# Optimization experiments

Hardware: AMD Instinct MI355X
Metric: run time of the kernel (lower is better)

## Reference

```python
import jax, jax.numpy as jnp
import numpy as np

B, N, S, D1, D2 = 8, 8192, 2048, 128, 256
MLP = [256, 128]
IN_CH = D1 + D2
EPS_INTERP = 1e-8
EPS_BN = 1e-5


def setup_inputs() -> dict:
    key = jax.random.key(0)
    ks = jax.random.split(key, 12)
    inp = {
        "xyz1": jax.random.normal(ks[0], (B, 3, N), dtype=jnp.float32),
        "xyz2": jax.random.normal(ks[1], (B, 3, S), dtype=jnp.float32),
        "points1": jax.random.normal(ks[2], (B, D1, N), dtype=jnp.float32),
        "points2": jax.random.normal(ks[3], (B, D2, S), dtype=jnp.float32),
    }
    # Conv1d(k=1) weights are [out, in]; BN has gamma/beta per channel.
    last = IN_CH
    for i, oc in enumerate(MLP):
        inp[f"W{i}"] = jax.random.normal(ks[4 + 2 * i], (oc, last), dtype=jnp.float32) * (1.0 / np.sqrt(last))
        inp[f"b{i}"] = jnp.zeros((oc,), dtype=jnp.float32)
        inp[f"g{i}"] = jnp.ones((oc,), dtype=jnp.float32)
        inp[f"be{i}"] = jnp.zeros((oc,), dtype=jnp.float32)
        last = oc
    return inp


def _interpolate(xyz1, xyz2, points2):
    # xyz1: [B,3,N] -> [B,N,3]; xyz2: [B,3,S] -> [B,S,3]; points2: [B,D2,S] -> [B,S,D2]
    x1 = jnp.transpose(xyz1, (0, 2, 1))
    x2 = jnp.transpose(xyz2, (0, 2, 1))
    p2 = jnp.transpose(points2, (0, 2, 1))
    # squared distances [B,N,S]
    dists = (jnp.sum(x1 * x1, -1)[:, :, None]
             - 2.0 * jnp.einsum("bnc,bsc->bns", x1, x2)
             + jnp.sum(x2 * x2, -1)[:, None, :])
    neg_d, idx = jax.lax.top_k(-dists, 3)         # 3 nearest neighbors
    d = -neg_d                                     # [B,N,3]
    recip = 1.0 / (d + EPS_INTERP)
    weight = recip / jnp.sum(recip, axis=2, keepdims=True)
    gathered = jax.vmap(lambda p, i: p[i])(p2, idx)   # [B,N,3,D2]
    return jnp.sum(gathered * weight[..., None], axis=2)  # [B,N,D2]


def _conv_bn_relu(x, W, b, g, be):
    # x: [B,C,N]; 1x1 conv == channel GEMM
    y = jnp.einsum("oc,bcn->bon", W, x) + b[None, :, None]
    mean = jnp.mean(y, axis=(0, 2), keepdims=True)
    var = jnp.mean((y - mean) ** 2, axis=(0, 2), keepdims=True)  # biased, torch BN train
    y = (y - mean) * jax.lax.rsqrt(var + EPS_BN)
    y = y * g[None, :, None] + be[None, :, None]
    return jax.nn.relu(y)


def reference(xyz1, xyz2, points1, points2, W0, b0, g0, be0, W1, b1, g1, be1):
    interp = _interpolate(xyz1, xyz2, points2)               # [B,N,D2]
    p1 = jnp.transpose(points1, (0, 2, 1))                    # [B,N,D1]
    new_points = jnp.concatenate([p1, interp], axis=-1)       # [B,N,D1+D2]
    new_points = jnp.transpose(new_points, (0, 2, 1))         # [B,D1+D2,N]
    new_points = _conv_bn_relu(new_points, W0, b0, g0, be0)
    new_points = _conv_bn_relu(new_points, W1, b1, g1, be1)
    return new_points
```

## Files before the change

### kernel.cpp

```cpp
#include <hip/hip_runtime.h>

typedef unsigned short ushort_t;
typedef __bf16 bf16x8 __attribute__((ext_vector_type(8)));
typedef float floatx4 __attribute__((ext_vector_type(4)));

#define B_ 8
#define N_ 8192
#define S_ 2048
#define D1_ 128
#define D2_ 256
#define INCH_ 384
#define M_ 65536

#define ASYNC_CP16(g, l)                                                  \
  __builtin_amdgcn_global_load_lds(                                       \
      (const __attribute__((address_space(1))) void*)(g),                 \
      (__attribute__((address_space(3))) void*)(l), 16, 0, 0)

constexpr size_t OFF_STATS = 0;
constexpr size_t OFF_W0B   = 8192;
constexpr size_t OFF_W1B   = 204800;
constexpr size_t OFF_X2P   = 270336;
constexpr size_t OFF_P2T   = 532480;
constexpr size_t OFF_XC    = 8921088;
constexpr size_t OFF_Y1    = 59252736;

__device__ __forceinline__ ushort_t f2bf(float f) {
  unsigned int u = __float_as_uint(f);
  unsigned int r = u + 0x7fffu + ((u >> 16) & 1u);
  return (ushort_t)(r >> 16);
}
__device__ __forceinline__ float bf2f(ushort_t h) {
  return __uint_as_float(((unsigned int)h) << 16);
}

__device__ __forceinline__ void ins3(float e, int s,
                                     float& c0, float& c1, float& c2,
                                     int& i0, int& i1, int& i2) {
  bool l0 = e < c0, l1 = e < c1, l2 = e < c2;
  float nf0 = fminf(e, c0);
  float nf1 = __builtin_amdgcn_fmed3f(e, c0, c1);
  float nf2 = __builtin_amdgcn_fmed3f(e, c1, c2);
  i2 = l1 ? i1 : (l2 ? s : i2);
  i1 = l0 ? i0 : (l1 ? s : i1);
  i0 = l0 ? s : i0;
  c0 = nf0; c1 = nf1; c2 = nf2;
}

__global__ __launch_bounds__(256) void k_prep(const float* __restrict__ W0,
                                              const float* __restrict__ W1,
                                              const float* __restrict__ xyz2,
                                              ushort_t* __restrict__ W0b,
                                              ushort_t* __restrict__ W1b,
                                              float4* __restrict__ x2p) {
  int i = blockIdx.x * 256 + threadIdx.x;
  if (i < 98304) {
    W0b[i] = f2bf(W0[i]);
  } else if (i < 131072) {
    W1b[i - 98304] = f2bf(W1[i - 98304]);
  } else {
    int idx = i - 131072;
    int b = idx >> 11, s = idx & (S_ - 1);
    const float* base = xyz2 + (size_t)b * 3 * S_;
    float x = base[s], y = base[S_ + s], z = base[2 * S_ + s];
    x2p[idx] = make_float4(x, y, z, 0.5f * (x * x + y * y + z * z));
  }
}

__global__ void k_tr_p2(const float* __restrict__ P2, ushort_t* __restrict__ p2t) {
  __shared__ float t[32][33];
  int b = blockIdx.z;
  int s0 = blockIdx.x * 32;
  int c0 = blockIdx.y * 32;
  int tx = threadIdx.x, ty = threadIdx.y;
#pragma unroll
  for (int j = 0; j < 4; j++) {
    int c = c0 + ty + j * 8;
    t[ty + j * 8][tx] = P2[((size_t)b * D2_ + c) * S_ + s0 + tx];
  }
  __syncthreads();
#pragma unroll
  for (int j = 0; j < 4; j++) {
    int s = s0 + ty + j * 8;
    p2t[((size_t)b * S_ + s) * D2_ + c0 + tx] = f2bf(t[tx][ty + j * 8]);
  }
}

__global__ void k_tr_p1(const float* __restrict__ P1, ushort_t* __restrict__ Xc) {
  __shared__ float t[32][33];
  int b = blockIdx.z;
  int n0 = blockIdx.x * 32;
  int c0 = blockIdx.y * 32;
  int tx = threadIdx.x, ty = threadIdx.y;
#pragma unroll
  for (int j = 0; j < 4; j++) {
    int c = c0 + ty + j * 8;
    t[ty + j * 8][tx] = P1[((size_t)b * D1_ + c) * N_ + n0 + tx];
  }
  __syncthreads();
#pragma unroll
  for (int j = 0; j < 4; j++) {
    int n = n0 + ty + j * 8;
    Xc[((size_t)b * N_ + n) * INCH_ + c0 + tx] = f2bf(t[tx][ty + j * 8]);
  }
}

__global__ __launch_bounds__(512, 8) void k_knn(const float* __restrict__ xyz1,
                                                const float4* __restrict__ x2p,
                                                const ushort_t* __restrict__ p2t,
                                                ushort_t* __restrict__ Xc) {
  __shared__ float4 xs[8 * 289];
  __shared__ float wsh[64 * 3];
  __shared__ int   ish[64 * 3];
  int t = threadIdx.x;
  int q0 = blockIdx.x * 64;
  int b = q0 >> 13;
  int n0 = q0 & (N_ - 1);
  for (int l = t; l < S_; l += 512)
    xs[(l >> 8) * 289 + (l & 255)] = x2p[(size_t)b * S_ + l];
  int sub = t & 7;
  int qg = t >> 3;
  int n = n0 + qg;
  float qx = xyz1[((size_t)b * 3 + 0) * N_ + n];
  float qy = xyz1[((size_t)b * 3 + 1) * N_ + n];
  float qz = xyz1[((size_t)b * 3 + 2) * N_ + n];
  float nrm1 = qx * qx + qy * qy + qz * qz;
  __syncthreads();
  const float4* bp = xs + sub * 289;
  float k0 = 3e38f, k1 = 3e38f, k2 = 3e38f, k3 = 3e38f;
#pragma unroll 4
  for (int i = 0; i < 256; ++i) {
    float4 P = bp[i];
    float e = fmaf(-qx, P.x, fmaf(-qy, P.y, fmaf(-qz, P.z, P.w)));
    float dd = fmaf(2.f, e, nrm1);
    unsigned int kb = (__float_as_uint(dd) & 0xFFFFFF00u) | (unsigned int)i;
    float k = __uint_as_float(kb);
    float n0_ = fminf(k, k0);
    float n1_ = __builtin_amdgcn_fmed3f(k, k0, k1);
    float n2_ = __builtin_amdgcn_fmed3f(k, k1, k2);
    float n3_ = __builtin_amdgcn_fmed3f(k, k2, k3);
    k0 = n0_; k1 = n1_; k2 = n2_; k3 = n3_;
  }
  float ed[4];
  int   si[4];
  {
    float kk[4] = {k0, k1, k2, k3};
#pragma unroll
    for (int c = 0; c < 4; ++c) {
      int loc = (int)(__float_as_uint(kk[c]) & 255u);
      float4 P = bp[loc];
      float e = fmaf(-qx, P.x, fmaf(-qy, P.y, fmaf(-qz, P.z, P.w)));
      ed[c] = fmaf(2.f, e, nrm1);
      si[c] = (sub << 8) + loc;
    }
  }
  float c0 = 3e38f, c1 = 3e38f, c2 = 3e38f;
  int i0 = 0, i1 = 0, i2 = 0;
#pragma unroll
  for (int c = 0; c < 4; ++c) ins3(ed[c], si[c], c0, c1, c2, i0, i1, i2);
#pragma unroll
  for (int d = 1; d < 8; d <<= 1) {
    float e0 = __shfl_xor(c0, d); int s0 = __shfl_xor(i0, d);
    float e1 = __shfl_xor(c1, d); int s1 = __shfl_xor(i1, d);
    float e2 = __shfl_xor(c2, d); int s2 = __shfl_xor(i2, d);
    ins3(e0, s0, c0, c1, c2, i0, i1, i2);
    ins3(e1, s1, c0, c1, c2, i0, i1, i2);
    ins3(e2, s2, c0, c1, c2, i0, i1, i2);
  }
  if (sub == 0) {
    float r0 = 1.f / (c0 + 1e-8f);
    float r1 = 1.f / (c1 + 1e-8f);
    float r2 = 1.f / (c2 + 1e-8f);
    float rs = 1.f / (r0 + r1 + r2);
    wsh[qg * 3 + 0] = r0 * rs; wsh[qg * 3 + 1] = r1 * rs; wsh[qg * 3 + 2] = r2 * rs;
    ish[qg * 3 + 0] = i0; ish[qg * 3 + 1] = i1; ish[qg * 3 + 2] = i2;
  }
  __syncthreads();
  int lane = t & 63, grp = t >> 6;
  size_t sbase2 = (size_t)b * S_;
#pragma unroll 2
  for (int it = 0; it < 8; ++it) {
    int ql = it * 8 + grp;
    int q = q0 + ql;
    float w0 = wsh[ql * 3 + 0], w1 = wsh[ql * 3 + 1], w2 = wsh[ql * 3 + 2];
    int j0 = ish[ql * 3 + 0], j1 = ish[ql * 3 + 1], j2 = ish[ql * 3 + 2];
    ushort4 a0 = *(const ushort4*)&p2t[(sbase2 + j0) * D2_ + lane * 4];
    ushort4 a1 = *(const ushort4*)&p2t[(sbase2 + j1) * D2_ + lane * 4];
    ushort4 a2 = *(const ushort4*)&p2t[(sbase2 + j2) * D2_ + lane * 4];
    ushort4 o;
    o.x = f2bf(w0 * bf2f(a0.x) + w1 * bf2f(a1.x) + w2 * bf2f(a2.x));
    o.y = f2bf(w0 * bf2f(a0.y) + w1 * bf2f(a1.y) + w2 * bf2f(a2.y));
    o.z = f2bf(w0 * bf2f(a0.z) + w1 * bf2f(a1.z) + w2 * bf2f(a2.z));
    o.w = f2bf(w0 * bf2f(a0.w) + w1 * bf2f(a1.w) + w2 * bf2f(a2.w));
    *(ushort4*)&Xc[(size_t)q * INCH_ + D1_ + lane * 4] = o;
  }
}

__global__ __launch_bounds__(512) void k_gemm1(const ushort_t* __restrict__ A,
                                               const ushort_t* __restrict__ Bw,
                                               ushort_t* __restrict__ Cc,
                                               float* __restrict__ sum,
                                               float* __restrict__ ssq) {
  __shared__ __align__(16) ushort_t As[128 * 32];
  __shared__ __align__(16) ushort_t Bs[256 * 32];
  const int tid = threadIdx.x;
  const int m0 = blockIdx.x * 128;
  const int wave = tid >> 6;
  const int wuni = __builtin_amdgcn_readfirstlane(wave);
  const int lane = tid & 63;
  const int quad = lane >> 4;
  const int l16 = lane & 15;
  const int wrow = (wave >> 2) * 64;
  const int wcol = (wave & 3) * 64;
  const int arow = tid >> 2, aseg = tid & 3;
  floatx4 acc[4][4];
#pragma unroll
  for (int i = 0; i < 4; i++)
#pragma unroll
    for (int j = 0; j < 4; j++) acc[i][j] = (floatx4){0.f, 0.f, 0.f, 0.f};

  for (int k0 = 0; k0 < INCH_; k0 += 32) {
    ASYNC_CP16(&A[(size_t)(m0 + arow) * INCH_ + k0 + aseg * 8], &As[wuni * 512]);
#pragma unroll
    for (int it = 0; it < 2; it++) {
      int l = tid + it * 512;
      int row = l >> 2, seg = l & 3;
      ASYNC_CP16(&Bw[(size_t)row * INCH_ + k0 + seg * 8], &Bs[it * 4096 + wuni * 512]);
    }
    __syncthreads();
    bf16x8 af[4], bfr[4];
#pragma unroll
    for (int mt = 0; mt < 4; mt++) af[mt] = *(const bf16x8*)&As[(wrow + mt * 16 + l16) * 32 + quad * 8];
#pragma unroll
    for (int nt = 0; nt < 4; nt++) bfr[nt] = *(const bf16x8*)&Bs[(wcol + nt * 16 + l16) * 32 + quad * 8];
#pragma unroll
    for (int mt = 0; mt < 4; mt++)
#pragma unroll
      for (int nt = 0; nt < 4; nt++)
        acc[mt][nt] = __builtin_amdgcn_mfma_f32_16x16x32_bf16(af[mt], bfr[nt], acc[mt][nt], 0, 0, 0);
    __syncthreads();
  }
#pragma unroll
  for (int mt = 0; mt < 4; mt++) {
#pragma unroll
    for (int i = 0; i < 4; i++) {
      int row = m0 + wrow + mt * 16 + quad * 4 + i;
#pragma unroll
      for (int nt = 0; nt < 4; nt++) {
        int col = wcol + nt * 16 + l16;
        Cc[(size_t)row * 256 + col] = f2bf(acc[mt][nt][i]);
      }
    }
  }
#pragma unroll
  for (int nt = 0; nt < 4; nt++) {
    float s = 0.f, s2 = 0.f;
#pragma unroll
    for (int mt = 0; mt < 4; mt++)
#pragma unroll
      for (int i = 0; i < 4; i++) {
        float v = acc[mt][nt][i];
        s += v;
        s2 = fmaf(v, v, s2);
      }
    s += __shfl_xor(s, 16);  s2 += __shfl_xor(s2, 16);
    s += __shfl_xor(s, 32);  s2 += __shfl_xor(s2, 32);
    if (quad == 0) {
      int col = wcol + nt * 16 + l16;
      atomicAdd(&sum[col], s);
      atomicAdd(&ssq[col], s2);
    }
  }
}

__global__ __launch_bounds__(256) void k_gemm2(const ushort_t* __restrict__ Y1,
                                               const ushort_t* __restrict__ Bw,
                                               const float* __restrict__ sum0,
                                               const float* __restrict__ ssq0,
                                               const float* __restrict__ g0,
                                               const float* __restrict__ be0,
                                               ushort_t* __restrict__ Cc,
                                               float* __restrict__ sum,
                                               float* __restrict__ ssq) {
  __shared__ __align__(16) ushort_t As[128 * 32];
  __shared__ __align__(16) ushort_t Bs[128 * 32];
  __shared__ float scs[256], shs[256];
  const int tid = threadIdx.x;
  const int m0 = blockIdx.x * 128;
  const int wave = tid >> 6;
  const int wuni = __builtin_amdgcn_readfirstlane(wave);
  const int lane = tid & 63;
  const int quad = lane >> 4;
  const int l16 = lane & 15;
  const int wrow = (wave >> 1) * 64;
  const int wcol = (wave & 1) * 64;
  {
    float mean = sum0[tid] * (1.f / 65536.f);
    float var = ssq0[tid] * (1.f / 65536.f) - mean * mean;
    float sc = rsqrtf(var + 1e-5f) * g0[tid];
    scs[tid] = sc;
    shs[tid] = be0[tid] - mean * sc;
  }
  floatx4 acc[4][4];
#pragma unroll
  for (int i = 0; i < 4; i++)
#pragma unroll
    for (int j = 0; j < 4; j++) acc[i][j] = (floatx4){0.f, 0.f, 0.f, 0.f};
  __syncthreads();

  for (int k0 = 0; k0 < 256; k0 += 32) {
#pragma unroll
    for (int it = 0; it < 2; it++) {
      int l = tid + it * 256;
      int row = l >> 2, seg = l & 3;
      ASYNC_CP16(&Bw[(size_t)row * 256 + k0 + seg * 8], &Bs[it * 2048 + wuni * 512]);
    }
#pragma unroll
    for (int it = 0; it < 2; it++) {
      int l = tid + it * 256;
      int row = l >> 2, seg = l & 3;
      ushort4 y01 = *(const ushort4*)&Y1[(size_t)(m0 + row) * 256 + k0 + seg * 8];
      ushort4 y23 = *(const ushort4*)&Y1[(size_t)(m0 + row) * 256 + k0 + seg * 8 + 4];
      int c = k0 + seg * 8;
      ushort4 o0, o1;
      o0.x = f2bf(fmaxf(fmaf(bf2f(y01.x), scs[c + 0], shs[c + 0]), 0.f));
      o0.y = f2bf(fmaxf(fmaf(bf2f(y01.y), scs[c + 1], shs[c + 1]), 0.f));
      o0.z = f2bf(fmaxf(fmaf(bf2f(y01.z), scs[c + 2], shs[c + 2]), 0.f));
      o0.w = f2bf(fmaxf(fmaf(bf2f(y01.w), scs[c + 3], shs[c + 3]), 0.f));
      o1.x = f2bf(fmaxf(fmaf(bf2f(y23.x), scs[c + 4], shs[c + 4]), 0.f));
      o1.y = f2bf(fmaxf(fmaf(bf2f(y23.y), scs[c + 5], shs[c + 5]), 0.f));
      o1.z = f2bf(fmaxf(fmaf(bf2f(y23.z), scs[c + 6], shs[c + 6]), 0.f));
      o1.w = f2bf(fmaxf(fmaf(bf2f(y23.w), scs[c + 7], shs[c + 7]), 0.f));
      *(ushort4*)&As[row * 32 + seg * 8] = o0;
      *(ushort4*)&As[row * 32 + seg * 8 + 4] = o1;
    }
    __syncthreads();
    bf16x8 af[4], bfr[4];
#pragma unroll
    for (int mt = 0; mt < 4; mt++) af[mt] = *(const bf16x8*)&As[(wrow + mt * 16 + l16) * 32 + quad * 8];
#pragma unroll
    for (int nt = 0; nt < 4; nt++) bfr[nt] = *(const bf16x8*)&Bs[(wcol + nt * 16 + l16) * 32 + quad * 8];
#pragma unroll
    for (int mt = 0; mt < 4; mt++)
#pragma unroll
      for (int nt = 0; nt < 4; nt++)
        acc[mt][nt] = __builtin_amdgcn_mfma_f32_16x16x32_bf16(af[mt], bfr[nt], acc[mt][nt], 0, 0, 0);
    __syncthreads();
  }
#pragma unroll
  for (int mt = 0; mt < 4; mt++) {
#pragma unroll
    for (int i = 0; i < 4; i++) {
      int row = m0 + wrow + mt * 16 + quad * 4 + i;
#pragma unroll
      for (int nt = 0; nt < 4; nt++) {
        int col = wcol + nt * 16 + l16;
        Cc[(size_t)row * 128 + col] = f2bf(acc[mt][nt][i]);
      }
    }
  }
#pragma unroll
  for (int nt = 0; nt < 4; nt++) {
    float s = 0.f, s2 = 0.f;
#pragma unroll
    for (int mt = 0; mt < 4; mt++)
#pragma unroll
      for (int i = 0; i < 4; i++) {
        float v = acc[mt][nt][i];
        s += v;
        s2 = fmaf(v, v, s2);
      }
    s += __shfl_xor(s, 16);  s2 += __shfl_xor(s2, 16);
    s += __shfl_xor(s, 32);  s2 += __shfl_xor(s2, 32);
    if (quad == 0) {
      int col = wcol + nt * 16 + l16;
      atomicAdd(&sum[col], s);
      atomicAdd(&ssq[col], s2);
    }
  }
}

__global__ __launch_bounds__(256) void k_out(const ushort_t* __restrict__ Y2,
                                             const float* __restrict__ sum1,
                                             const float* __restrict__ ssq1,
                                             const float* __restrict__ g1,
                                             const float* __restrict__ be1,
                                             float* __restrict__ out) {
  __shared__ float t[64 * 129];
  __shared__ float sc1[128], sh1[128];
  int tid = threadIdx.x;
  int p0 = blockIdx.x * 64;
  int b = p0 >> 13;
  int n0 = p0 & (N_ - 1);
  if (tid < 128) {
    float mean = sum1[tid] * (1.f / 65536.f);
    float var = ssq1[tid] * (1.f / 65536.f) - mean * mean;
    float sc = rsqrtf(var + 1e-5f) * g1[tid];
    sc1[tid] = sc;
    sh1[tid] = be1[tid] - mean * sc;
  }
#pragma unroll
  for (int it = 0; it < 8; it++) {
    int idx = it * 256 + tid;
    int r = idx >> 5, c4 = (idx & 31) * 4;
    ushort4 v = *(const ushort4*)&Y2[(size_t)(p0 + r) * 128 + c4];
    t[r * 129 + c4 + 0] = bf2f(v.x);
    t[r * 129 + c4 + 1] = bf2f(v.y);
    t[r * 129 + c4 + 2] = bf2f(v.z);
    t[r * 129 + c4 + 3] = bf2f(v.w);
  }
  __syncthreads();
#pragma unroll
  for (int it = 0; it < 32; it++) {
    int idx = it * 256 + tid;
    int j = idx & 63, c = idx >> 6;
    float v = fmaxf(fmaf(t[j * 129 + c], sc1[c], sh1[c]), 0.f);
    out[((size_t)(b * 128 + c)) * N_ + n0 + j] = v;
  }
}

extern "C" void kernel_launch(void* const* d_in, const int* in_sizes, int n_in,
                              void* d_out, int out_size, void* d_ws, size_t ws_size,
                              hipStream_t stream) {
  const float* xyz1    = (const float*)d_in[0];
  const float* xyz2    = (const float*)d_in[1];
  const float* points1 = (const float*)d_in[2];
  const float* points2 = (const float*)d_in[3];
  const float* W0 = (const float*)d_in[4];
  const float* g0 = (const float*)d_in[6];
  const float* be0 = (const float*)d_in[7];
  const float* W1 = (const float*)d_in[8];
  const float* g1 = (const float*)d_in[10];
  const float* be1 = (const float*)d_in[11];
  float* out = (float*)d_out;
  char* ws = (char*)d_ws;

  float* sum0   = (float*)(ws + OFF_STATS);
  float* ssq0   = sum0 + 256;
  float* sum1   = sum0 + 512;
  float* ssq1   = sum0 + 640;
  ushort_t* W0b = (ushort_t*)(ws + OFF_W0B);
  ushort_t* W1b = (ushort_t*)(ws + OFF_W1B);
  float4* x2p   = (float4*)(ws + OFF_X2P);
  ushort_t* p2t = (ushort_t*)(ws + OFF_P2T);
  ushort_t* Xc  = (ushort_t*)(ws + OFF_XC);
  ushort_t* Y1b = (ushort_t*)(ws + OFF_Y1);
  ushort_t* Y2b = (ushort_t*)(ws + OFF_XC);

  hipMemsetAsync(ws + OFF_STATS, 0, 6144, stream);
  k_prep<<<576, 256, 0, stream>>>(W0, W1, xyz2, W0b, W1b, x2p);
  k_tr_p2<<<dim3(64, 8, 8), dim3(32, 8), 0, stream>>>(points2, p2t);
  k_tr_p1<<<dim3(256, 4, 8), dim3(32, 8), 0, stream>>>(points1, Xc);
  k_knn<<<1024, 512, 0, stream>>>(xyz1, x2p, p2t, Xc);
  k_gemm1<<<512, 512, 0, stream>>>(Xc, W0b, Y1b, sum0, ssq0);
  k_gemm2<<<512, 256, 0, stream>>>(Y1b, W1b, sum0, ssq0, g0, be0, Y2b, sum1, ssq1);
  k_out<<<1024, 256, 0, stream>>>(Y2b, sum1, ssq1, g1, be1, out);
}
```

Before: 253.6 us.

## Fuse second GEMM with final BN/ReLU output via grid-wide atomic barrier

```diff
diff --git a/kernel.cpp b/kernel.cpp
--- a/kernel.cpp
+++ b/kernel.cpp
@@ -11,6 +11,7 @@
 #define D2_ 256
 #define INCH_ 384
 #define M_ 65536
+#define G2_NBLK 512
 
 #define ASYNC_CP16(g, l)                                                  \
   __builtin_amdgcn_global_load_lds(                                       \
@@ -26,9 +27,10 @@
 constexpr size_t OFF_Y1    = 59252736;
 
 __device__ __forceinline__ ushort_t f2bf(float f) {
-  unsigned int u = __float_as_uint(f);
-  unsigned int r = u + 0x7fffu + ((u >> 16) & 1u);
-  return (ushort_t)(r >> 16);
+  __bf16 h = (__bf16)f;
+  union { __bf16 h; ushort_t u; } v;
+  v.h = h;
+  return v.u;
 }
 __device__ __forceinline__ float bf2f(ushort_t h) {
   return __uint_as_float(((unsigned int)h) << 16);
@@ -273,20 +275,27 @@
   }
 }
 
-__global__ __launch_bounds__(256) void k_gemm2(const ushort_t* __restrict__ Y1,
-                                               const ushort_t* __restrict__ Bw,
-                                               const float* __restrict__ sum0,
-                                               const float* __restrict__ ssq0,
-                                               const float* __restrict__ g0,
-                                               const float* __restrict__ be0,
-                                               ushort_t* __restrict__ Cc,
-                                               float* __restrict__ sum,
-                                               float* __restrict__ ssq) {
-  __shared__ __align__(16) ushort_t As[128 * 32];
-  __shared__ __align__(16) ushort_t Bs[128 * 32];
+__global__ __launch_bounds__(256, 2) void k_gemm2o(const ushort_t* __restrict__ Y1,
+                                                   const ushort_t* __restrict__ Bw,
+                                                   const float* __restrict__ sum0,
+                                                   const float* __restrict__ ssq0,
+                                                   const float* __restrict__ g0,
+                                                   const float* __restrict__ be0,
+                                                   const float* __restrict__ g1,
+                                                   const float* __restrict__ be1,
+                                                   float* __restrict__ sum1,
+                                                   float* __restrict__ ssq1,
+                                                   unsigned int* __restrict__ barcnt,
+                                                   float* __restrict__ out) {
+  __shared__ __align__(16) char ubuf[64 * 129 * 4];
   __shared__ float scs[256], shs[256];
+  ushort_t* As = (ushort_t*)ubuf;
+  ushort_t* Bs = (ushort_t*)(ubuf + 8192);
+  float* tb = (float*)ubuf;
   const int tid = threadIdx.x;
   const int m0 = blockIdx.x * 128;
+  const int b = m0 >> 13;
+  const int n0 = m0 & (N_ - 1);
   const int wave = tid >> 6;
   const int wuni = __builtin_amdgcn_readfirstlane(wave);
   const int lane = tid & 63;
@@ -348,18 +357,6 @@
     __syncthreads();
   }
 #pragma unroll
-  for (int mt = 0; mt < 4; mt++) {
-#pragma unroll
-    for (int i = 0; i < 4; i++) {
-      int row = m0 + wrow + mt * 16 + quad * 4 + i;
-#pragma unroll
-      for (int nt = 0; nt < 4; nt++) {
-        int col = wcol + nt * 16 + l16;
-        Cc[(size_t)row * 128 + col] = f2bf(acc[mt][nt][i]);
-      }
-    }
-  }
-#pragma unroll
   for (int nt = 0; nt < 4; nt++) {
     float s = 0.f, s2 = 0.f;
 #pragma unroll
@@ -374,48 +371,57 @@
     s += __shfl_xor(s, 32);  s2 += __shfl_xor(s2, 32);
     if (quad == 0) {
       int col = wcol + nt * 16 + l16;
-      atomicAdd(&sum[col], s);
-      atomicAdd(&ssq[col], s2);
-    }
-  }
-}
-
-__global__ __launch_bounds__(256) void k_out(const ushort_t* __restrict__ Y2,
-                                             const float* __restrict__ sum1,
-                                             const float* __restrict__ ssq1,
-                                             const float* __restrict__ g1,
-                                             const float* __restrict__ be1,
-                                             float* __restrict__ out) {
-  __shared__ float t[64 * 129];
-  __shared__ float sc1[128], sh1[128];
-  int tid = threadIdx.x;
-  int p0 = blockIdx.x * 64;
-  int b = p0 >> 13;
-  int n0 = p0 & (N_ - 1);
+      atomicAdd(&sum1[col], s);
+      atomicAdd(&ssq1[col], s2);
+    }
+  }
+
+  __syncthreads();
+  if (tid == 0) {
+    __hip_atomic_fetch_add(barcnt, 1u, __ATOMIC_ACQ_REL, __HIP_MEMORY_SCOPE_AGENT);
+    while (__hip_atomic_load(barcnt, __ATOMIC_ACQUIRE, __HIP_MEMORY_SCOPE_AGENT)
+           < (unsigned)G2_NBLK) {
+      __builtin_amdgcn_s_sleep(8);
+    }
+  }
+  __syncthreads();
+
   if (tid < 128) {
-    float mean = sum1[tid] * (1.f / 65536.f);
-    float var = ssq1[tid] * (1.f / 65536.f) - mean * mean;
+    float sv = __hip_atomic_load(&sum1[tid], __ATOMIC_RELAXED, __HIP_MEMORY_SCOPE_AGENT);
+    float qv = __hip_atomic_load(&ssq1[tid], __ATOMIC_RELAXED, __HIP_MEMORY_SCOPE_AGENT);
+    float mean = sv * (1.f / 65536.f);
+    float var = qv * (1.f / 65536.f) - mean * mean;
     float sc = rsqrtf(var + 1e-5f) * g1[tid];
-    sc1[tid] = sc;
-    sh1[tid] = be1[tid] - mean * sc;
-  }
-#pragma unroll
-  for (int it = 0; it < 8; it++) {
-    int idx = it * 256 + tid;
-    int r = idx >> 5, c4 = (idx & 31) * 4;
-    ushort4 v = *(const ushort4*)&Y2[(size_t)(p0 + r) * 128 + c4];
-    t[r * 129 + c4 + 0] = bf2f(v.x);
-    t[r * 129 + c4 + 1] = bf2f(v.y);
-    t[r * 129 + c4 + 2] = bf2f(v.z);
-    t[r * 129 + c4 + 3] = bf2f(v.w);
-  }
-  __syncthreads();
-#pragma unroll
-  for (int it = 0; it < 32; it++) {
-    int idx = it * 256 + tid;
-    int j = idx & 63, c = idx >> 6;
-    float v = fmaxf(fmaf(t[j * 129 + c], sc1[c], sh1[c]), 0.f);
-    out[((size_t)(b * 128 + c)) * N_ + n0 + j] = v;
+    scs[tid] = sc;
+    shs[tid] = be1[tid] - mean * sc;
+  }
+  __syncthreads();
+
+  const int mych = wrow >> 6;
+#pragma unroll
+  for (int c2 = 0; c2 < 2; ++c2) {
+    if (mych == c2) {
+#pragma unroll
+      for (int mt = 0; mt < 4; mt++)
+#pragma unroll
+        for (int i = 0; i < 4; i++) {
+          int rl = mt * 16 + quad * 4 + i;
+#pragma unroll
+          for (int nt = 0; nt < 4; nt++) {
+            int col = wcol + nt * 16 + l16;
+            float v = fmaxf(fmaf(acc[mt][nt][i], scs[col], shs[col]), 0.f);
+            tb[rl * 129 + col] = v;
+          }
+        }
+    }
+    __syncthreads();
+#pragma unroll
+    for (int it = 0; it < 32; ++it) {
+      int idx = it * 256 + tid;
+      int j = idx & 63, c = idx >> 6;
+      out[((size_t)(b * 128 + c)) * N_ + n0 + c2 * 64 + j] = tb[j * 129 + c];
+    }
+    __syncthreads();
   }
 }
 
@@ -439,13 +445,13 @@
   float* ssq0   = sum0 + 256;
   float* sum1   = sum0 + 512;
   float* ssq1   = sum0 + 640;
+  unsigned int* barcnt = (unsigned int*)(sum0 + 768);
   ushort_t* W0b = (ushort_t*)(ws + OFF_W0B);
   ushort_t* W1b = (ushort_t*)(ws + OFF_W1B);
   float4* x2p   = (float4*)(ws + OFF_X2P);
   ushort_t* p2t = (ushort_t*)(ws + OFF_P2T);
   ushort_t* Xc  = (ushort_t*)(ws + OFF_XC);
   ushort_t* Y1b = (ushort_t*)(ws + OFF_Y1);
-  ushort_t* Y2b = (ushort_t*)(ws + OFF_XC);
 
   hipMemsetAsync(ws + OFF_STATS, 0, 6144, stream);
   k_prep<<<576, 256, 0, stream>>>(W0, W1, xyz2, W0b, W1b, x2p);
@@ -453,6 +459,6 @@
   k_tr_p1<<<dim3(256, 4, 8), dim3(32, 8), 0, stream>>>(points1, Xc);
   k_knn<<<1024, 512, 0, stream>>>(xyz1, x2p, p2t, Xc);
   k_gemm1<<<512, 512, 0, stream>>>(Xc, W0b, Y1b, sum0, ssq0);
-  k_gemm2<<<512, 256, 0, stream>>>(Y1b, W1b, sum0, ssq0, g0, be0, Y2b, sum1, ssq1);
-  k_out<<<1024, 256, 0, stream>>>(Y2b, sum1, ssq1, g1, be1, out);
-}
+  k_gemm2o<<<G2_NBLK, 256, 0, stream>>>(Y1b, W1b, sum0, ssq0, g0, be0,
+                                        g1, be1, sum1, ssq1, barcnt, out);
+}
```

Measured after the change: 269.4 us. 6.2% more time.
